# Kernel tuning notes

Measured on AMD Instinct MI355X. Metric: run time of the kernel, lower is better.

## Reference

```python
import jax, jax.numpy as jnp
import numpy as np

B, L, H, N, O = 64, 512, 768, 50, 768
ALPHA = 0.3  # leaky relu slope in GAT
NEG_INF = -9e15


def _position_encoding(n, d):
    # standard sinusoidal PE, shape [n, d]
    pos = jnp.arange(n, dtype=jnp.float32)[:, None]              # [n,1]
    div = jnp.exp(jnp.arange(0, d, 2, dtype=jnp.float32) * (-np.log(10000.0) / d))  # [d/2]
    ang = pos * div[None, :]                                     # [n, d/2]
    return jnp.stack([jnp.sin(ang), jnp.cos(ang)], axis=-1).reshape(n, d)


def _gat_layer(x, adj, W, b, a, ab):
    # Dense GAT layer. Original builds an [N,N,2F] concat tensor then applies
    # linear a; mathematically identical to splitting a into src/dst halves.
    Wh = x @ W + b                                               # [N,F]
    Fdim = Wh.shape[-1]
    a_src = Wh @ a[:Fdim]                                        # [N]
    a_dst = Wh @ a[Fdim:]                                        # [N]
    e = jax.nn.leaky_relu(a_src[:, None] + a_dst[None, :] + ab, negative_slope=ALPHA)
    att = jax.nn.softmax(jnp.where(adj > 0, e, NEG_INF), axis=1)  # rows sum to 1
    return att @ Wh                                              # [N,F]


def setup_inputs() -> dict:
    key = jax.random.key(0)
    ks = jax.random.split(key, 16)
    s = 1.0 / np.sqrt(H)
    utter_embedding = jax.random.normal(ks[0], (B, L, H), jnp.float32)
    cls_ids = jnp.sort(jax.random.randint(ks[1], (B, N), 0, L), axis=1).astype(jnp.int32)
    adj = jax.random.randint(ks[2], (B, N, N), 0, 2).astype(jnp.int32)
    adj = adj | jnp.eye(N, dtype=jnp.int32)  # ensure self loops so softmax rows are valid
    return {
        "utter_embedding": utter_embedding,
        "cls_ids": cls_ids,
        "adj": adj,
        # GAT head 0 (concat=True)
        "W1": jax.random.normal(ks[3], (H, H), jnp.float32) * s,
        "b1": jnp.zeros((H,), jnp.float32),
        "a1": jax.random.normal(ks[4], (2 * H,), jnp.float32) * s,
        "ab1": jnp.zeros((), jnp.float32),
        # GAT out layer (concat=False)
        "W2": jax.random.normal(ks[5], (H, H), jnp.float32) * s,
        "b2": jnp.zeros((H,), jnp.float32),
        "a2": jax.random.normal(ks[6], (2 * H,), jnp.float32) * s,
        "ab2": jnp.zeros((), jnp.float32),
        # Attention pooling over utterances
        "Wa": jax.random.normal(ks[7], (H, H), jnp.float32) * s,
        "ba": jnp.zeros((H,), jnp.float32),
        "v": jax.random.normal(ks[8], (H,), jnp.float32) * s,
        # Final linear
        "Wl": jax.random.normal(ks[9], (H, O), jnp.float32) * s,
        "bl": jnp.zeros((O,), jnp.float32),
    }


def reference(utter_embedding, cls_ids, adj, W1, b1, a1, ab1, W2, b2, a2, ab2,
              Wa, ba, v, Wl, bl):
    pe = _position_encoding(N, H)                                # [N,H]

    def per_dialogue(emb, ids, A):
        # gather [CLS] utterance embeddings: index_select
        x = jnp.take(emb, ids, axis=0)                           # [N,H]
        x = x + pe                                               # position encoder
        # GAT: 1 head concat -> elu, out layer -> elu, residual
        h = jax.nn.elu(_gat_layer(x, A, W1, b1, a1, ab1))
        h = jax.nn.elu(_gat_layer(h, A, W2, b2, a2, ab2)) + x    # residual per GAT.forward
        # attention pooling over N utterances
        scores = jax.nn.softmax(jnp.tanh(h @ Wa + ba) @ v, axis=0)  # [N]
        return scores @ h                                        # [H]

    dialogue = jax.vmap(per_dialogue)(utter_embedding, cls_ids, adj)  # [B,H]
    return dialogue @ Wl + bl                                    # [B,O]
```

## Files before the change

### kernel.cpp

```cpp
#include <hip/hip_runtime.h>
#include <hip/hip_bf16.h>
#include <math.h>

typedef __attribute__((ext_vector_type(8))) short bf16x8;
typedef __attribute__((ext_vector_type(4))) float f32x4;
typedef __attribute__((ext_vector_type(4))) unsigned short u16x4;

constexpr int Bn = 64;
constexpr int Ln = 512;
constexpr int Hd = 768;
constexpr int Nn = 50;
constexpr int On = 768;
constexpr int RP = 64;

__device__ __forceinline__ f32x4 MFMA(bf16x8 a, bf16x8 b, f32x4 c) {
  return __builtin_amdgcn_mfma_f32_16x16x32_bf16(a, b, c, 0, 0, 0);
}
__device__ __forceinline__ unsigned short f2bb(float v) {
  __hip_bfloat16 h = __float2bfloat16(v);
  return *(unsigned short*)&h;
}
__device__ __forceinline__ void gload16(const void* g, void* l) {
  __builtin_amdgcn_global_load_lds(
      (const __attribute__((address_space(1))) void*)g,
      (__attribute__((address_space(3))) void*)l, 16, 0, 0);
}

struct PrepArgs {
  const float* src[4];
  __hip_bfloat16* dst[4];
  const float* emb;
  const int* ids;
  float* xres;
  __hip_bfloat16* xb;
  float* aux;
};

__global__ __launch_bounds__(256) void prep_kernel(PrepArgs a) {
  int bx = blockIdx.x;
  if (bx < 2304) {
    __shared__ float tile[32][33];
    int job = bx / 576, t = bx % 576;
    const float* W = a.src[job];
    __hip_bfloat16* Wt = a.dst[job];
    int tx = (t % 24) * 32, ty = (t / 24) * 32;
    int c = threadIdx.x & 31, r0 = threadIdx.x >> 5;
    for (int r = r0; r < 32; r += 8)
      tile[r][c] = W[(size_t)(tx + r) * Hd + ty + c];
    __syncthreads();
    for (int r = r0; r < 32; r += 8)
      Wt[(size_t)(ty + r) * Hd + tx + c] = __float2bfloat16(tile[c][r]);
  } else if (bx < 6400) {
    int bn = bx - 2304;
    int b = bn >> 6, i = bn & 63;
    __hip_bfloat16* xbo = a.xb + (size_t)bn * Hd;
    float* xro = a.xres + (size_t)bn * Hd;
    if (i < Nn) {
      int id = a.ids[b * Nn + i];
      const float* src = a.emb + ((size_t)b * Ln + id) * Hd;
      const float kLog = 9.210340371976184f / (float)Hd;
      for (int h = threadIdx.x; h < Hd; h += 256) {
        float freq = expf(-(float)(h & ~1) * kLog);
        float ang = (float)i * freq;
        float v = src[h] + ((h & 1) ? cosf(ang) : sinf(ang));
        xbo[h] = __float2bfloat16(v);
        xro[h] = v;
      }
    } else {
      for (int h = threadIdx.x; h < Hd; h += 256) {
        xbo[h] = __float2bfloat16(0.f);
        xro[h] = 0.f;
      }
    }
  } else {
    int idx = (bx - 6400) * 256 + threadIdx.x;
    if (idx < 5 * Bn * RP) a.aux[idx] = 0.f;
  }
}

template <int EPI>
__global__ __launch_bounds__(512) void gemm_kernel(
    const __hip_bfloat16* __restrict__ A, const __hip_bfloat16* __restrict__ Bt,
    const float* __restrict__ bias, __hip_bfloat16* __restrict__ WhT,
    const float* __restrict__ avec, float* __restrict__ o1,
    float* __restrict__ o2) {
  __shared__ __hip_bfloat16 As[2][64][64];
  __shared__ __hip_bfloat16 Bs[2][64][64];
  int tid = threadIdx.x;
  int wave = tid >> 6, lane = tid & 63;
  int lr = lane & 15, lq = lane >> 4;
  int wr = wave >> 1, wc = wave & 1;
  int b = blockIdx.x, col0 = blockIdx.y * 64;
  int row0 = b * RP;

  int srow = wave * 8 + (lane >> 3);
  int swz = ((lane & 7) ^ (lane >> 3)) * 8;
  const __hip_bfloat16* Ap = A + (size_t)(row0 + srow) * Hd + swz;
  const __hip_bfloat16* Bp = Bt + (size_t)(col0 + srow) * Hd + swz;
  char* AsB = (char*)As;
  char* BsB = (char*)Bs;
  int ldsw = wave * 1024;

  auto stage = [&](int buf, int kt) {
    gload16(Ap + kt, AsB + buf * 8192 + ldsw);
    gload16(Bp + kt, BsB + buf * 8192 + ldsw);
  };

  f32x4 acc[2] = {};
  stage(0, 0);
  __syncthreads();
  int cur = 0;
  int arow = wr * 16 + lr;
  int s7 = lr & 7;
  int c0 = (lq ^ s7) * 16;
  int c1 = ((4 + lq) ^ s7) * 16;
  for (int kt = 64; kt < Hd; kt += 64) {
    stage(cur ^ 1, kt);
    const char* Ab = AsB + cur * 8192 + arow * 128;
    bf16x8 af0 = *(const bf16x8*)(Ab + c0);
    bf16x8 af1 = *(const bf16x8*)(Ab + c1);
#pragma unroll
    for (int ct = 0; ct < 2; ++ct) {
      const char* Bb = BsB + cur * 8192 + (wc * 32 + ct * 16 + lr) * 128;
      acc[ct] = MFMA(af0, *(const bf16x8*)(Bb + c0), acc[ct]);
      acc[ct] = MFMA(af1, *(const bf16x8*)(Bb + c1), acc[ct]);
    }
    __syncthreads();
    cur ^= 1;
  }
  {
    const char* Ab = AsB + cur * 8192 + arow * 128;
    bf16x8 af0 = *(const bf16x8*)(Ab + c0);
    bf16x8 af1 = *(const bf16x8*)(Ab + c1);
#pragma unroll
    for (int ct = 0; ct < 2; ++ct) {
      const char* Bb = BsB + cur * 8192 + (wc * 32 + ct * 16 + lr) * 128;
      acc[ct] = MFMA(af0, *(const bf16x8*)(Bb + c0), acc[ct]);
      acc[ct] = MFMA(af1, *(const bf16x8*)(Bb + c1), acc[ct]);
    }
  }
  int lrow0 = wr * 16 + lq * 4;
  if (EPI == 0) {
    float ps[4] = {}, pd[4] = {};
#pragma unroll
    for (int ct = 0; ct < 2; ++ct) {
      int gc = col0 + wc * 32 + ct * 16 + lr;
      float bv = bias[gc];
      float a_s = avec[gc], a_d = avec[Hd + gc];
      u16x4 pk;
#pragma unroll
      for (int r = 0; r < 4; ++r) {
        float v = acc[ct][r] + bv;
        pk[r] = f2bb(v);
        ps[r] += v * a_s;
        pd[r] += v * a_d;
      }
      *(u16x4*)(WhT + ((size_t)b * Hd + gc) * RP + lrow0) = pk;
    }
#pragma unroll
    for (int off = 8; off; off >>= 1)
#pragma unroll
      for (int r = 0; r < 4; ++r) {
        ps[r] += __shfl_xor(ps[r], off);
        pd[r] += __shfl_xor(pd[r], off);
      }
    if (lr == 0)
#pragma unroll
      for (int r = 0; r < 4; ++r) {
        int row = lrow0 + r;
        if (row < Nn) {
          atomicAdd(&o1[b * RP + row], ps[r]);
          atomicAdd(&o2[b * RP + row], pd[r]);
        }
      }
  } else {
    float pr[4] = {};
#pragma unroll
    for (int ct = 0; ct < 2; ++ct) {
      int gc = col0 + wc * 32 + ct * 16 + lr;
      float bv = bias[gc];
      float vv_ = avec[gc];
#pragma unroll
      for (int r = 0; r < 4; ++r) pr[r] += tanhf(acc[ct][r] + bv) * vv_;
    }
#pragma unroll
    for (int off = 8; off; off >>= 1)
#pragma unroll
      for (int r = 0; r < 4; ++r) pr[r] += __shfl_xor(pr[r], off);
    if (lr == 0)
#pragma unroll
      for (int r = 0; r < 4; ++r) {
        int row = lrow0 + r;
        if (row < Nn) atomicAdd(&o1[b * RP + row], pr[r]);
      }
  }
}

template <int LAYER>
__global__ __launch_bounds__(256) void attf_kernel(
    const float* __restrict__ ssrc, const float* __restrict__ sdst,
    const int* __restrict__ adj, const float* __restrict__ ab,
    const __hip_bfloat16* __restrict__ WhT, const float* __restrict__ xres,
    float* __restrict__ hf, __hip_bfloat16* __restrict__ hb) {
  int b = blockIdx.x / 12, cg = blockIdx.x % 12;
  __shared__ float attL[Nn * 52];
  __shared__ __hip_bfloat16 attB[64 * 72];
  int tid = threadIdx.x;
  float abv = ab[0];
  for (int i = tid; i < 64 * 72; i += 256) attB[i] = __float2bfloat16(0.f);
  for (int idx = tid; idx < Nn * Nn; idx += 256) {
    int i = idx / Nn, j = idx - i * Nn;
    float t = ssrc[b * RP + i] + sdst[b * RP + j] + abv;
    t = t > 0.f ? t : 0.3f * t;
    attL[i * 52 + j] = (adj[(size_t)b * Nn * Nn + idx] > 0) ? t : -9.0e15f;
  }
  __syncthreads();
  if (tid < Nn) {
    float m = -3.0e38f;
    for (int j = 0; j < Nn; ++j) m = fmaxf(m, attL[tid * 52 + j]);
    float s = 0.f;
    for (int j = 0; j < Nn; ++j) {
      float p = expf(attL[tid * 52 + j] - m);
      attL[tid * 52 + j] = p;
      s += p;
    }
    float inv = 1.f / s;
    for (int j = 0; j < Nn; ++j) attL[tid * 52 + j] *= inv;
  }
  __syncthreads();
  for (int idx = tid; idx < Nn * Nn; idx += 256) {
    int i = idx / Nn, j = idx - i * Nn;
    attB[i * 72 + j] = __float2bfloat16(attL[i * 52 + j]);
  }
  __syncthreads();

  int w = tid >> 6, lane = tid & 63, lr = lane & 15, lq = lane >> 4;
  bf16x8 a0 = *(const bf16x8*)&attB[(w * 16 + lr) * 72 + lq * 8];
  bf16x8 a1 = *(const bf16x8*)&attB[(w * 16 + lr) * 72 + 32 + lq * 8];
#pragma unroll
  for (int s = 0; s < 4; ++s) {
    int gc = cg * 64 + s * 16 + lr;
    const __hip_bfloat16* Bp = WhT + ((size_t)b * Hd + gc) * RP + lq * 8;
    f32x4 acc = {};
    acc = MFMA(a0, *(const bf16x8*)Bp, acc);
    acc = MFMA(a1, *(const bf16x8*)(Bp + 32), acc);
#pragma unroll
    for (int r = 0; r < 4; ++r) {
      float v = acc[r];
      v = v > 0.f ? v : expf(v) - 1.f;
      size_t off = ((size_t)b * RP + w * 16 + lq * 4 + r) * Hd + gc;
      if (LAYER == 2) {
        v += xres[off];
        hf[off] = v;
      }
      hb[off] = __float2bfloat16(v);
    }
  }
}

__global__ __launch_bounds__(256) void poolfinal_kernel(
    const float* __restrict__ sraw, const float* __restrict__ h2,
    const __hip_bfloat16* __restrict__ Wlt, const float* __restrict__ bl,
    float* __restrict__ out) {
  int b = blockIdx.x / 3, q = blockIdx.x % 3;
  __shared__ float sc[Nn];
  __shared__ float ds[Hd];
  if (threadIdx.x < 64) {
    int j = threadIdx.x;
    float e = (j < Nn) ? sraw[b * RP + j] : -3.0e38f;
    float m = e;
#pragma unroll
    for (int off = 32; off; off >>= 1) m = fmaxf(m, __shfl_xor(m, off));
    float p = (j < Nn) ? expf(e - m) : 0.f;
    float s = p;
#pragma unroll
    for (int off = 32; off; off >>= 1) s += __shfl_xor(s, off);
    if (j < Nn) sc[j] = p / s;
  }
  __syncthreads();
  for (int h = threadIdx.x; h < Hd; h += 256) {
    float a = 0.f;
#pragma unroll 10
    for (int j = 0; j < Nn; ++j) a += sc[j] * h2[((size_t)b * RP + j) * Hd + h];
    ds[h] = a;
  }
  __syncthreads();
  {
    int o = q * 256 + threadIdx.x;
    float acc = bl[o];
    const uint4* wr = (const uint4*)(Wlt + (size_t)o * Hd);
    for (int kk = 0; kk < Hd / 8; ++kk) {
      union { uint4 u; unsigned short s[8]; } w;
      w.u = wr[kk];
#pragma unroll
      for (int t = 0; t < 8; ++t)
        acc += ds[kk * 8 + t] * __uint_as_float((unsigned)w.s[t] << 16);
    }
    out[(size_t)b * On + o] = acc;
  }
}

extern "C" void kernel_launch(void* const* d_in, const int* in_sizes, int n_in,
                              void* d_out, int out_size, void* d_ws, size_t ws_size,
                              hipStream_t stream) {
  const float* emb = (const float*)d_in[0];
  const int* ids = (const int*)d_in[1];
  const int* adj = (const int*)d_in[2];
  const float* W1 = (const float*)d_in[3];
  const float* b1 = (const float*)d_in[4];
  const float* a1 = (const float*)d_in[5];
  const float* ab1 = (const float*)d_in[6];
  const float* W2 = (const float*)d_in[7];
  const float* b2 = (const float*)d_in[8];
  const float* a2 = (const float*)d_in[9];
  const float* ab2 = (const float*)d_in[10];
  const float* Wa = (const float*)d_in[11];
  const float* ba = (const float*)d_in[12];
  const float* vv = (const float*)d_in[13];
  const float* Wl = (const float*)d_in[14];
  const float* bl = (const float*)d_in[15];
  float* out = (float*)d_out;

  char* p = (char*)d_ws;
  auto alloc = [&](size_t bytes) {
    char* r = p;
    p += (bytes + 255) & ~(size_t)255;
    return r;
  };
  __hip_bfloat16* Wt1 = (__hip_bfloat16*)alloc((size_t)Hd * Hd * 2);
  __hip_bfloat16* Wt2 = (__hip_bfloat16*)alloc((size_t)Hd * Hd * 2);
  __hip_bfloat16* Wta = (__hip_bfloat16*)alloc((size_t)Hd * Hd * 2);
  __hip_bfloat16* Wlt = (__hip_bfloat16*)alloc((size_t)Hd * On * 2);
  float* aux = (float*)alloc((size_t)5 * Bn * RP * 4);
  float* ssrc1 = aux;
  float* sdst1 = aux + Bn * RP;
  float* ssrc2 = aux + 2 * Bn * RP;
  float* sdst2 = aux + 3 * Bn * RP;
  float* sraw = aux + 4 * Bn * RP;
  __hip_bfloat16* xb = (__hip_bfloat16*)alloc((size_t)Bn * RP * Hd * 2);
  float* xres = (float*)alloc((size_t)Bn * RP * Hd * 4);
  __hip_bfloat16* WhT1 = (__hip_bfloat16*)alloc((size_t)Bn * Hd * RP * 2);
  __hip_bfloat16* WhT2 = (__hip_bfloat16*)alloc((size_t)Bn * Hd * RP * 2);
  __hip_bfloat16* h1b = (__hip_bfloat16*)alloc((size_t)Bn * RP * Hd * 2);
  __hip_bfloat16* h2b = (__hip_bfloat16*)alloc((size_t)Bn * RP * Hd * 2);
  float* h2f = (float*)alloc((size_t)Bn * RP * Hd * 4);

  PrepArgs pa;
  pa.src[0] = W1; pa.src[1] = W2; pa.src[2] = Wa; pa.src[3] = Wl;
  pa.dst[0] = Wt1; pa.dst[1] = Wt2; pa.dst[2] = Wta; pa.dst[3] = Wlt;
  pa.emb = emb; pa.ids = ids; pa.xres = xres; pa.xb = xb; pa.aux = aux;
  prep_kernel<<<6480, 256, 0, stream>>>(pa);

  dim3 ggrid(Bn, Hd / 64);
  dim3 agrid(Bn * 12);
  dim3 pgrid(Bn * 3);

  gemm_kernel<0><<<ggrid, 512, 0, stream>>>(xb, Wt1, b1, WhT1, a1, ssrc1, sdst1);
  attf_kernel<1><<<agrid, 256, 0, stream>>>(ssrc1, sdst1, adj, ab1, WhT1,
                                            nullptr, nullptr, h1b);
  gemm_kernel<0><<<ggrid, 512, 0, stream>>>(h1b, Wt2, b2, WhT2, a2, ssrc2, sdst2);
  attf_kernel<2><<<agrid, 256, 0, stream>>>(ssrc2, sdst2, adj, ab2, WhT2, xres,
                                            h2f, h2b);
  gemm_kernel<1><<<ggrid, 512, 0, stream>>>(h2b, Wta, ba, nullptr, vv, sraw,
                                            nullptr);
  poolfinal_kernel<<<pgrid, 256, 0, stream>>>(sraw, h2f, Wlt, bl, out);
}
```

Baseline: 260.3 us.

## Fuse attention and pooling into GEMM kernels via last-block-done counters

Merges each GAT attention kernel and the final pooling kernel into the preceding GEMM kernel. Each of the 12 column blocks of a dialogue bumps a per-dialogue atomic counter, and the last one to finish runs the softmax/aggregation or pooling/linear epilogue. This removes three kernel launches and their gaps. In exchange, the epilogue work for each dialogue runs in a single block instead of being spread over 12 (or 3) blocks, which serializes it and leaves a tail where few blocks are active.

New measurement: 348.4 us. 33.8% more time.

```diff
diff --git a/kernel.cpp b/kernel.cpp
--- a/kernel.cpp
+++ b/kernel.cpp
@@ -1,6 +1,7 @@
 #include <hip/hip_runtime.h>
 #include <hip/hip_bf16.h>
 #include <math.h>
+#include <string.h>
 
 typedef __attribute__((ext_vector_type(8))) short bf16x8;
 typedef __attribute__((ext_vector_type(4))) float f32x4;
@@ -12,6 +13,8 @@
 constexpr int Nn = 50;
 constexpr int On = 768;
 constexpr int RP = 64;
+
+constexpr int AUXW = 5 * Bn * RP + 3 * Bn;
 
 __device__ __forceinline__ f32x4 MFMA(bf16x8 a, bf16x8 b, f32x4 c) {
   return __builtin_amdgcn_mfma_f32_16x16x32_bf16(a, b, c, 0, 0, 0);
@@ -74,18 +77,30 @@
     }
   } else {
     int idx = (bx - 6400) * 256 + threadIdx.x;
-    if (idx < 5 * Bn * RP) a.aux[idx] = 0.f;
+    if (idx < AUXW) a.aux[idx] = 0.f;
   }
 }
 
-template <int EPI>
-__global__ __launch_bounds__(512) void gemm_kernel(
-    const __hip_bfloat16* __restrict__ A, const __hip_bfloat16* __restrict__ Bt,
-    const float* __restrict__ bias, __hip_bfloat16* __restrict__ WhT,
-    const float* __restrict__ avec, float* __restrict__ o1,
-    float* __restrict__ o2) {
-  __shared__ __hip_bfloat16 As[2][64][64];
-  __shared__ __hip_bfloat16 Bs[2][64][64];
+struct GArgs {
+  const __hip_bfloat16 *A, *Bt;
+  const float *bias, *avec;
+  __hip_bfloat16* WhT;
+  float *o1, *o2;
+  const int* adj;
+  const float* ab;
+  const float* xres;
+  float* hf;
+  __hip_bfloat16* hb;
+  const float* h2;
+  const __hip_bfloat16* Wlt;
+  const float* bl;
+  float* out;
+  int* tick;
+};
+
+template <int EPI, int POST>
+__global__ __launch_bounds__(512) void gfuse_kernel(GArgs g) {
+  __shared__ __align__(16) char arena[33024];
   int tid = threadIdx.x;
   int wave = tid >> 6, lane = tid & 63;
   int lr = lane & 15, lq = lane >> 4;
@@ -93,210 +108,215 @@
   int b = blockIdx.x, col0 = blockIdx.y * 64;
   int row0 = b * RP;
 
-  int srow = wave * 8 + (lane >> 3);
-  int swz = ((lane & 7) ^ (lane >> 3)) * 8;
-  const __hip_bfloat16* Ap = A + (size_t)(row0 + srow) * Hd + swz;
-  const __hip_bfloat16* Bp = Bt + (size_t)(col0 + srow) * Hd + swz;
-  char* AsB = (char*)As;
-  char* BsB = (char*)Bs;
-  int ldsw = wave * 1024;
-
-  auto stage = [&](int buf, int kt) {
-    gload16(Ap + kt, AsB + buf * 8192 + ldsw);
-    gload16(Bp + kt, BsB + buf * 8192 + ldsw);
-  };
-
-  f32x4 acc[2] = {};
-  stage(0, 0);
+  {
+    char* AsB = arena;
+    char* BsB = arena + 16384;
+    int srow = wave * 8 + (lane >> 3);
+    int swz = ((lane & 7) ^ (lane >> 3)) * 8;
+    const __hip_bfloat16* Ap = g.A + (size_t)(row0 + srow) * Hd + swz;
+    const __hip_bfloat16* Bp = g.Bt + (size_t)(col0 + srow) * Hd + swz;
+    int ldsw = wave * 1024;
+    auto stage = [&](int buf, int kt) {
+      gload16(Ap + kt, AsB + buf * 8192 + ldsw);
+      gload16(Bp + kt, BsB + buf * 8192 + ldsw);
+    };
+    f32x4 acc[2] = {};
+    stage(0, 0);
+    __syncthreads();
+    int cur = 0;
+    int arow = wr * 16 + lr;
+    int s7 = lr & 7;
+    int c0 = (lq ^ s7) * 16;
+    int c1 = ((4 + lq) ^ s7) * 16;
+    for (int kt = 64; kt < Hd; kt += 64) {
+      stage(cur ^ 1, kt);
+      const char* Ab = AsB + cur * 8192 + arow * 128;
+      bf16x8 af0 = *(const bf16x8*)(Ab + c0);
+      bf16x8 af1 = *(const bf16x8*)(Ab + c1);
+#pragma unroll
+      for (int ct = 0; ct < 2; ++ct) {
+        const char* Bb = BsB + cur * 8192 + (wc * 32 + ct * 16 + lr) * 128;
+        acc[ct] = MFMA(af0, *(const bf16x8*)(Bb + c0), acc[ct]);
+        acc[ct] = MFMA(af1, *(const bf16x8*)(Bb + c1), acc[ct]);
+      }
+      __syncthreads();
+      cur ^= 1;
+    }
+    {
+      const char* Ab = AsB + cur * 8192 + arow * 128;
+      bf16x8 af0 = *(const bf16x8*)(Ab + c0);
+      bf16x8 af1 = *(const bf16x8*)(Ab + c1);
+#pragma unroll
+      for (int ct = 0; ct < 2; ++ct) {
+        const char* Bb = BsB + cur * 8192 + (wc * 32 + ct * 16 + lr) * 128;
+        acc[ct] = MFMA(af0, *(const bf16x8*)(Bb + c0), acc[ct]);
+        acc[ct] = MFMA(af1, *(const bf16x8*)(Bb + c1), acc[ct]);
+      }
+    }
+    int lrow0 = wr * 16 + lq * 4;
+    if (EPI == 0) {
+      float ps[4] = {}, pd[4] = {};
+#pragma unroll
+      for (int ct = 0; ct < 2; ++ct) {
+        int gc = col0 + wc * 32 + ct * 16 + lr;
+        float bv = g.bias[gc];
+        float a_s = g.avec[gc], a_d = g.avec[Hd + gc];
+        u16x4 pk;
+#pragma unroll
+        for (int r = 0; r < 4; ++r) {
+          float v = acc[ct][r] + bv;
+          pk[r] = f2bb(v);
+          ps[r] += v * a_s;
+          pd[r] += v * a_d;
+        }
+        unsigned long long pv;
+        __builtin_memcpy(&pv, &pk, 8);
+        __hip_atomic_store(
+            (unsigned long long*)(g.WhT + ((size_t)b * Hd + gc) * RP + lrow0),
+            pv, __ATOMIC_RELAXED, __HIP_MEMORY_SCOPE_AGENT);
+      }
+#pragma unroll
+      for (int off = 8; off; off >>= 1)
+#pragma unroll
+        for (int r = 0; r < 4; ++r) {
+          ps[r] += __shfl_xor(ps[r], off);
+          pd[r] += __shfl_xor(pd[r], off);
+        }
+      if (lr == 0)
+#pragma unroll
+        for (int r = 0; r < 4; ++r) {
+          int row = lrow0 + r;
+          if (row < Nn) {
+            atomicAdd(&g.o1[b * RP + row], ps[r]);
+            atomicAdd(&g.o2[b * RP + row], pd[r]);
+          }
+        }
+    } else {
+      float pr[4] = {};
+#pragma unroll
+      for (int ct = 0; ct < 2; ++ct) {
+        int gc = col0 + wc * 32 + ct * 16 + lr;
+        float bv = g.bias[gc];
+        float vv_ = g.avec[gc];
+#pragma unroll
+        for (int r = 0; r < 4; ++r) pr[r] += tanhf(acc[ct][r] + bv) * vv_;
+      }
+#pragma unroll
+      for (int off = 8; off; off >>= 1)
+#pragma unroll
+        for (int r = 0; r < 4; ++r) pr[r] += __shfl_xor(pr[r], off);
+      if (lr == 0)
+#pragma unroll
+        for (int r = 0; r < 4; ++r) {
+          int row = lrow0 + r;
+          if (row < Nn) atomicAdd(&g.o1[b * RP + row], pr[r]);
+        }
+    }
+  }
+
   __syncthreads();
-  int cur = 0;
-  int arow = wr * 16 + lr;
-  int s7 = lr & 7;
-  int c0 = (lq ^ s7) * 16;
-  int c1 = ((4 + lq) ^ s7) * 16;
-  for (int kt = 64; kt < Hd; kt += 64) {
-    stage(cur ^ 1, kt);
-    const char* Ab = AsB + cur * 8192 + arow * 128;
-    bf16x8 af0 = *(const bf16x8*)(Ab + c0);
-    bf16x8 af1 = *(const bf16x8*)(Ab + c1);
-#pragma unroll
-    for (int ct = 0; ct < 2; ++ct) {
-      const char* Bb = BsB + cur * 8192 + (wc * 32 + ct * 16 + lr) * 128;
-      acc[ct] = MFMA(af0, *(const bf16x8*)(Bb + c0), acc[ct]);
-      acc[ct] = MFMA(af1, *(const bf16x8*)(Bb + c1), acc[ct]);
-    }
-    __syncthreads();
-    cur ^= 1;
-  }
-  {
-    const char* Ab = AsB + cur * 8192 + arow * 128;
-    bf16x8 af0 = *(const bf16x8*)(Ab + c0);
-    bf16x8 af1 = *(const bf16x8*)(Ab + c1);
-#pragma unroll
-    for (int ct = 0; ct < 2; ++ct) {
-      const char* Bb = BsB + cur * 8192 + (wc * 32 + ct * 16 + lr) * 128;
-      acc[ct] = MFMA(af0, *(const bf16x8*)(Bb + c0), acc[ct]);
-      acc[ct] = MFMA(af1, *(const bf16x8*)(Bb + c1), acc[ct]);
-    }
-  }
-  int lrow0 = wr * 16 + lq * 4;
-  if (EPI == 0) {
-    float ps[4] = {}, pd[4] = {};
-#pragma unroll
-    for (int ct = 0; ct < 2; ++ct) {
-      int gc = col0 + wc * 32 + ct * 16 + lr;
-      float bv = bias[gc];
-      float a_s = avec[gc], a_d = avec[Hd + gc];
-      u16x4 pk;
-#pragma unroll
-      for (int r = 0; r < 4; ++r) {
-        float v = acc[ct][r] + bv;
-        pk[r] = f2bb(v);
-        ps[r] += v * a_s;
-        pd[r] += v * a_d;
-      }
-      *(u16x4*)(WhT + ((size_t)b * Hd + gc) * RP + lrow0) = pk;
-    }
-#pragma unroll
-    for (int off = 8; off; off >>= 1)
-#pragma unroll
-      for (int r = 0; r < 4; ++r) {
-        ps[r] += __shfl_xor(ps[r], off);
-        pd[r] += __shfl_xor(pd[r], off);
-      }
-    if (lr == 0)
-#pragma unroll
-      for (int r = 0; r < 4; ++r) {
-        int row = lrow0 + r;
-        if (row < Nn) {
-          atomicAdd(&o1[b * RP + row], ps[r]);
-          atomicAdd(&o2[b * RP + row], pd[r]);
-        }
-      }
-  } else {
-    float pr[4] = {};
-#pragma unroll
-    for (int ct = 0; ct < 2; ++ct) {
-      int gc = col0 + wc * 32 + ct * 16 + lr;
-      float bv = bias[gc];
-      float vv_ = avec[gc];
-#pragma unroll
-      for (int r = 0; r < 4; ++r) pr[r] += tanhf(acc[ct][r] + bv) * vv_;
-    }
-#pragma unroll
-    for (int off = 8; off; off >>= 1)
-#pragma unroll
-      for (int r = 0; r < 4; ++r) pr[r] += __shfl_xor(pr[r], off);
-    if (lr == 0)
-#pragma unroll
-      for (int r = 0; r < 4; ++r) {
-        int row = lrow0 + r;
-        if (row < Nn) atomicAdd(&o1[b * RP + row], pr[r]);
-      }
-  }
-}
-
-template <int LAYER>
-__global__ __launch_bounds__(256) void attf_kernel(
-    const float* __restrict__ ssrc, const float* __restrict__ sdst,
-    const int* __restrict__ adj, const float* __restrict__ ab,
-    const __hip_bfloat16* __restrict__ WhT, const float* __restrict__ xres,
-    float* __restrict__ hf, __hip_bfloat16* __restrict__ hb) {
-  int b = blockIdx.x / 12, cg = blockIdx.x % 12;
-  __shared__ float attL[Nn * 52];
-  __shared__ __hip_bfloat16 attB[64 * 72];
-  int tid = threadIdx.x;
-  float abv = ab[0];
-  for (int i = tid; i < 64 * 72; i += 256) attB[i] = __float2bfloat16(0.f);
-  for (int idx = tid; idx < Nn * Nn; idx += 256) {
-    int i = idx / Nn, j = idx - i * Nn;
-    float t = ssrc[b * RP + i] + sdst[b * RP + j] + abv;
-    t = t > 0.f ? t : 0.3f * t;
-    attL[i * 52 + j] = (adj[(size_t)b * Nn * Nn + idx] > 0) ? t : -9.0e15f;
+  int* flag = (int*)arena;
+  if (tid == 0) {
+    int old = __hip_atomic_fetch_add(&g.tick[b], 1, __ATOMIC_ACQ_REL,
+                                     __HIP_MEMORY_SCOPE_AGENT);
+    *flag = (old == 11) ? 1 : 0;
   }
   __syncthreads();
-  if (tid < Nn) {
-    float m = -3.0e38f;
-    for (int j = 0; j < Nn; ++j) m = fmaxf(m, attL[tid * 52 + j]);
-    float s = 0.f;
-    for (int j = 0; j < Nn; ++j) {
-      float p = expf(attL[tid * 52 + j] - m);
-      attL[tid * 52 + j] = p;
-      s += p;
-    }
-    float inv = 1.f / s;
-    for (int j = 0; j < Nn; ++j) attL[tid * 52 + j] *= inv;
-  }
+  bool take = (*flag != 0);
   __syncthreads();
-  for (int idx = tid; idx < Nn * Nn; idx += 256) {
-    int i = idx / Nn, j = idx - i * Nn;
-    attB[i * 72 + j] = __float2bfloat16(attL[i * 52 + j]);
-  }
+  if (!take) return;
+  if (tid == 0) __builtin_amdgcn_fence(__ATOMIC_ACQUIRE, "agent");
   __syncthreads();
 
-  int w = tid >> 6, lane = tid & 63, lr = lane & 15, lq = lane >> 4;
-  bf16x8 a0 = *(const bf16x8*)&attB[(w * 16 + lr) * 72 + lq * 8];
-  bf16x8 a1 = *(const bf16x8*)&attB[(w * 16 + lr) * 72 + 32 + lq * 8];
-#pragma unroll
-  for (int s = 0; s < 4; ++s) {
-    int gc = cg * 64 + s * 16 + lr;
-    const __hip_bfloat16* Bp = WhT + ((size_t)b * Hd + gc) * RP + lq * 8;
-    f32x4 acc = {};
-    acc = MFMA(a0, *(const bf16x8*)Bp, acc);
-    acc = MFMA(a1, *(const bf16x8*)(Bp + 32), acc);
-#pragma unroll
-    for (int r = 0; r < 4; ++r) {
-      float v = acc[r];
-      v = v > 0.f ? v : expf(v) - 1.f;
-      size_t off = ((size_t)b * RP + w * 16 + lq * 4 + r) * Hd + gc;
-      if (LAYER == 2) {
-        v += xres[off];
-        hf[off] = v;
-      }
-      hb[off] = __float2bfloat16(v);
-    }
-  }
-}
-
-__global__ __launch_bounds__(256) void poolfinal_kernel(
-    const float* __restrict__ sraw, const float* __restrict__ h2,
-    const __hip_bfloat16* __restrict__ Wlt, const float* __restrict__ bl,
-    float* __restrict__ out) {
-  int b = blockIdx.x / 3, q = blockIdx.x % 3;
-  __shared__ float sc[Nn];
-  __shared__ float ds[Hd];
-  if (threadIdx.x < 64) {
-    int j = threadIdx.x;
-    float e = (j < Nn) ? sraw[b * RP + j] : -3.0e38f;
-    float m = e;
-#pragma unroll
-    for (int off = 32; off; off >>= 1) m = fmaxf(m, __shfl_xor(m, off));
-    float p = (j < Nn) ? expf(e - m) : 0.f;
-    float s = p;
-#pragma unroll
-    for (int off = 32; off; off >>= 1) s += __shfl_xor(s, off);
-    if (j < Nn) sc[j] = p / s;
-  }
-  __syncthreads();
-  for (int h = threadIdx.x; h < Hd; h += 256) {
-    float a = 0.f;
+  if (POST == 1 || POST == 2) {
+    float* attL = (float*)arena;
+    __hip_bfloat16* attB = (__hip_bfloat16*)(arena + Nn * 52 * 4);
+    float abv = g.ab[0];
+    for (int i = tid; i < 64 * 72; i += 512) attB[i] = __float2bfloat16(0.f);
+    for (int idx = tid; idx < Nn * Nn; idx += 512) {
+      int i = idx / Nn, j = idx - i * Nn;
+      float t = g.o1[b * RP + i] + g.o2[b * RP + j] + abv;
+      t = t > 0.f ? t : 0.3f * t;
+      attL[i * 52 + j] = (g.adj[(size_t)b * Nn * Nn + idx] > 0) ? t : -9.0e15f;
+    }
+    __syncthreads();
+    if (tid < Nn) {
+      float m = -3.0e38f;
+      for (int j = 0; j < Nn; ++j) m = fmaxf(m, attL[tid * 52 + j]);
+      float s = 0.f;
+      for (int j = 0; j < Nn; ++j) {
+        float p = expf(attL[tid * 52 + j] - m);
+        attL[tid * 52 + j] = p;
+        s += p;
+      }
+      float inv = 1.f / s;
+      for (int j = 0; j < Nn; ++j) attL[tid * 52 + j] *= inv;
+    }
+    __syncthreads();
+    for (int idx = tid; idx < Nn * Nn; idx += 512) {
+      int i = idx / Nn, j = idx - i * Nn;
+      attB[i * 72 + j] = __float2bfloat16(attL[i * 52 + j]);
+    }
+    __syncthreads();
+    int strip = wave & 3;
+    int half = wave >> 2;
+    bf16x8 a0 = *(const bf16x8*)&attB[(strip * 16 + lr) * 72 + lq * 8];
+    bf16x8 a1 = *(const bf16x8*)&attB[(strip * 16 + lr) * 72 + 32 + lq * 8];
+#pragma unroll
+    for (int s = 0; s < 24; ++s) {
+      int gc = half * 384 + s * 16 + lr;
+      const __hip_bfloat16* Bp = g.WhT + ((size_t)b * Hd + gc) * RP + lq * 8;
+      f32x4 acc = {};
+      acc = MFMA(a0, *(const bf16x8*)Bp, acc);
+      acc = MFMA(a1, *(const bf16x8*)(Bp + 32), acc);
+#pragma unroll
+      for (int r = 0; r < 4; ++r) {
+        float v = acc[r];
+        v = v > 0.f ? v : expf(v) - 1.f;
+        size_t off = ((size_t)b * RP + strip * 16 + lq * 4 + r) * Hd + gc;
+        if (POST == 2) {
+          v += g.xres[off];
+          g.hf[off] = v;
+        }
+        g.hb[off] = __float2bfloat16(v);
+      }
+    }
+  } else if (POST == 3) {
+    float* sc = (float*)arena;
+    float* ds = (float*)(arena + 256);
+    if (tid < 64) {
+      int j = tid;
+      float e = (j < Nn) ? g.o1[b * RP + j] : -3.0e38f;
+      float m = e;
+#pragma unroll
+      for (int off = 32; off; off >>= 1) m = fmaxf(m, __shfl_xor(m, off));
+      float p = (j < Nn) ? expf(e - m) : 0.f;
+      float s = p;
+#pragma unroll
+      for (int off = 32; off; off >>= 1) s += __shfl_xor(s, off);
+      if (j < Nn) sc[j] = p / s;
+    }
+    __syncthreads();
+    for (int h = tid; h < Hd; h += 512) {
+      float a = 0.f;
 #pragma unroll 10
-    for (int j = 0; j < Nn; ++j) a += sc[j] * h2[((size_t)b * RP + j) * Hd + h];
-    ds[h] = a;
-  }
-  __syncthreads();
-  {
-    int o = q * 256 + threadIdx.x;
-    float acc = bl[o];
-    const uint4* wr = (const uint4*)(Wlt + (size_t)o * Hd);
-    for (int kk = 0; kk < Hd / 8; ++kk) {
-      union { uint4 u; unsigned short s[8]; } w;
-      w.u = wr[kk];
-#pragma unroll
-      for (int t = 0; t < 8; ++t)
-        acc += ds[kk * 8 + t] * __uint_as_float((unsigned)w.s[t] << 16);
-    }
-    out[(size_t)b * On + o] = acc;
+      for (int j = 0; j < Nn; ++j)
+        a += sc[j] * g.h2[((size_t)b * RP + j) * Hd + h];
+      ds[h] = a;
+    }
+    __syncthreads();
+    for (int o = tid; o < On; o += 512) {
+      float acc = g.bl[o];
+      const uint4* wrp = (const uint4*)(g.Wlt + (size_t)o * Hd);
+      for (int kk = 0; kk < Hd / 8; ++kk) {
+        union { uint4 u; unsigned short s[8]; } w;
+        w.u = wrp[kk];
+#pragma unroll
+        for (int t = 0; t < 8; ++t)
+          acc += ds[kk * 8 + t] * __uint_as_float((unsigned)w.s[t] << 16);
+      }
+      g.out[(size_t)b * On + o] = acc;
+    }
   }
 }
 
@@ -331,12 +351,13 @@
   __hip_bfloat16* Wt2 = (__hip_bfloat16*)alloc((size_t)Hd * Hd * 2);
   __hip_bfloat16* Wta = (__hip_bfloat16*)alloc((size_t)Hd * Hd * 2);
   __hip_bfloat16* Wlt = (__hip_bfloat16*)alloc((size_t)Hd * On * 2);
-  float* aux = (float*)alloc((size_t)5 * Bn * RP * 4);
+  float* aux = (float*)alloc((size_t)AUXW * 4);
   float* ssrc1 = aux;
   float* sdst1 = aux + Bn * RP;
   float* ssrc2 = aux + 2 * Bn * RP;
   float* sdst2 = aux + 3 * Bn * RP;
   float* sraw = aux + 4 * Bn * RP;
+  int* tick = (int*)(aux + 5 * Bn * RP);
   __hip_bfloat16* xb = (__hip_bfloat16*)alloc((size_t)Bn * RP * Hd * 2);
   float* xres = (float*)alloc((size_t)Bn * RP * Hd * 4);
   __hip_bfloat16* WhT1 = (__hip_bfloat16*)alloc((size_t)Bn * Hd * RP * 2);
@@ -349,19 +370,28 @@
   pa.src[0] = W1; pa.src[1] = W2; pa.src[2] = Wa; pa.src[3] = Wl;
   pa.dst[0] = Wt1; pa.dst[1] = Wt2; pa.dst[2] = Wta; pa.dst[3] = Wlt;
   pa.emb = emb; pa.ids = ids; pa.xres = xres; pa.xb = xb; pa.aux = aux;
-  prep_kernel<<<6480, 256, 0, stream>>>(pa);
+  prep_kernel<<<6481, 256, 0, stream>>>(pa);
 
   dim3 ggrid(Bn, Hd / 64);
-  dim3 agrid(Bn * 12);
-  dim3 pgrid(Bn * 3);
-
-  gemm_kernel<0><<<ggrid, 512, 0, stream>>>(xb, Wt1, b1, WhT1, a1, ssrc1, sdst1);
-  attf_kernel<1><<<agrid, 256, 0, stream>>>(ssrc1, sdst1, adj, ab1, WhT1,
-                                            nullptr, nullptr, h1b);
-  gemm_kernel<0><<<ggrid, 512, 0, stream>>>(h1b, Wt2, b2, WhT2, a2, ssrc2, sdst2);
-  attf_kernel<2><<<agrid, 256, 0, stream>>>(ssrc2, sdst2, adj, ab2, WhT2, xres,
-                                            h2f, h2b);
-  gemm_kernel<1><<<ggrid, 512, 0, stream>>>(h2b, Wta, ba, nullptr, vv, sraw,
-                                            nullptr);
-  poolfinal_kernel<<<pgrid, 256, 0, stream>>>(sraw, h2f, Wlt, bl, out);
-}
+
+  GArgs g1 = {};
+  g1.A = xb; g1.Bt = Wt1; g1.bias = b1; g1.avec = a1;
+  g1.WhT = WhT1; g1.o1 = ssrc1; g1.o2 = sdst1;
+  g1.adj = adj; g1.ab = ab1; g1.hb = h1b;
+  g1.tick = tick;
+  gfuse_kernel<0, 1><<<ggrid, 512, 0, stream>>>(g1);
+
+  GArgs g2 = {};
+  g2.A = h1b; g2.Bt = Wt2; g2.bias = b2; g2.avec = a2;
+  g2.WhT = WhT2; g2.o1 = ssrc2; g2.o2 = sdst2;
+  g2.adj = adj; g2.ab = ab2; g2.xres = xres; g2.hf = h2f; g2.hb = h2b;
+  g2.tick = tick + Bn;
+  gfuse_kernel<0, 2><<<ggrid, 512, 0, stream>>>(g2);
+
+  GArgs g3 = {};
+  g3.A = h2b; g3.Bt = Wta; g3.bias = ba; g3.avec = vv;
+  g3.o1 = sraw;
+  g3.h2 = h2f; g3.Wlt = Wlt; g3.bl = bl; g3.out = out;
+  g3.tick = tick + 2 * Bn;
+  gfuse_kernel<1, 3><<<ggrid, 512, 0, stream>>>(g3);
+}
```
